# Kernel tuning notes

Hardware: AMD Instinct MI355X
Metric: run time of the kernel (lower is better)

## Reference

```python
import jax, jax.numpy as jnp
import numpy as np

B, N, D = 8, 2048, 1024
DQ, DV = 1024, 1024


def setup_inputs() -> dict:
    key = jax.random.key(0)
    ks = jax.random.split(key, 7)
    s = 1.0 / np.sqrt(D)
    return {
        "x": jax.random.normal(ks[0], (B, N, D), dtype=jnp.float32),
        "Wq": jax.random.uniform(ks[1], (D, DQ), jnp.float32, -s, s),
        "bq": jax.random.uniform(ks[2], (DQ,), jnp.float32, -s, s),
        "Wk": jax.random.uniform(ks[3], (D, DQ), jnp.float32, -s, s),
        "bk": jax.random.uniform(ks[4], (DQ,), jnp.float32, -s, s),
        "Wv": jax.random.uniform(ks[5], (D, DV), jnp.float32, -s, s),
        "bv": jax.random.uniform(ks[6], (DV,), jnp.float32, -s, s),
    }


def reference(x, Wq, bq, Wk, bk, Wv, bv):
    # Linear projections (nn.Linear: x @ W + b)
    Q = jnp.einsum("bnd,dq->bnq", x, Wq) + bq  # [B,N,DQ]
    K = jnp.einsum("bnd,dq->bnq", x, Wk) + bk  # [B,N,DQ]
    V = jnp.einsum("bnd,dv->bnv", x, Wv) + bv  # [B,N,DV]
    # NOTE: original forward does NOT apply the 1/sqrt(dk) scaling.
    scores = jnp.einsum("bnq,bmq->bnm", Q, K)  # [B,N,N]
    attn = jax.nn.softmax(scores, axis=-1)
    out = jnp.einsum("bnm,bmv->bnv", attn, V)  # [B,N,DV]
    return out
```

## Files before the change

kernel.cpp:

```cpp
#include <hip/hip_runtime.h>
#include <hip/hip_bf16.h>
#include <stdint.h>


typedef _Float16 f16;
typedef _Float16 f16x8 __attribute__((ext_vector_type(8)));
typedef _Float16 f16x4 __attribute__((ext_vector_type(4)));
typedef float f32x4 __attribute__((ext_vector_type(4)));

typedef __attribute__((address_space(3))) void lds_void;
typedef const __attribute__((address_space(1))) void gbl_void;

__device__ __forceinline__ void async16(void* l, const void* g) {
    __builtin_amdgcn_global_load_lds(
        reinterpret_cast<gbl_void*>(reinterpret_cast<uintptr_t>(g)),
        reinterpret_cast<lds_void*>(reinterpret_cast<uintptr_t>(l)),
        16, 0, 0);
}

__global__ __launch_bounds__(256) void cast_f32_f16(const float* __restrict__ x,
                                                    f16* __restrict__ y) {
    long i = (long)blockIdx.x * 256 + threadIdx.x;
    float4 v = reinterpret_cast<const float4*>(x)[i];
    f16x4 o = {(f16)v.x, (f16)v.y, (f16)v.z, (f16)v.w};
    reinterpret_cast<f16x4*>(y)[i] = o;
}

__global__ __launch_bounds__(256) void transpose_cast3(const float* __restrict__ W0,
                                                       const float* __restrict__ W1,
                                                       const float* __restrict__ W2,
                                                       f16* __restrict__ wt) {
    const float* W = blockIdx.z == 0 ? W0 : blockIdx.z == 1 ? W1 : W2;
    f16* o = wt + (long)blockIdx.z * 1024 * 1024;
    __shared__ float tile[32][33];
    int c0 = blockIdx.x * 32, r0 = blockIdx.y * 32;
    int tx = threadIdx.x, ty = threadIdx.y;
#pragma unroll
    for (int i = ty; i < 32; i += 8) tile[i][tx] = W[(long)(r0 + i) * 1024 + c0 + tx];
    __syncthreads();
#pragma unroll
    for (int i = ty; i < 32; i += 8) o[(long)(c0 + i) * 1024 + r0 + tx] = (f16)tile[tx][i];
}

template <int MODE>
__global__ __launch_bounds__(512, 2) void gemm256(
    const f16* __restrict__ A, const f16* __restrict__ Bm,
    f16* __restrict__ o16, float* __restrict__ o32,
    const float* __restrict__ bq, const float* __restrict__ bk,
    const float* __restrict__ bv,
    f16* __restrict__ Qo, f16* __restrict__ Ko, f16* __restrict__ Vto) {
    constexpr int LDA = MODE == 2 ? 2048 : 1024;
    constexpr int LDB = MODE == 2 ? 2048 : 1024;
    constexpr int NT = (MODE == 2 ? 2048 : 1024) / 64;

    __shared__ f16 sm[65536];
    char* smb = (char*)sm;

    const int tid = threadIdx.x;
    const int lane = tid & 63;
    const int wv = tid >> 6;
    const int wmi = wv >> 2;
    const int wni = wv & 3;

    const int L = blockIdx.x;
    long mBase, nBase, oOff = 0;
    int nx = 0;
    if (MODE == 0) {
        const int xcd = L & 7, j = L >> 3;
        nx = j >> 3;
        mBase = (long)(xcd * 8 + (j & 7)) * 256;
        nBase = (long)nx * 256;
    } else if (MODE == 1) {
        const int b = L & 7, j = L >> 3;
        mBase = (long)(j & 7) * 256;
        nBase = (long)(j >> 3) * 256;
        A += (long)b * 2048 * 1024;
        Bm += (long)b * 2048 * 1024;
        oOff = (long)b * 2048 * 2048;
    } else {
        const int b = L & 7, j = L >> 3;
        mBase = (long)(j & 7) * 256;
        nBase = (long)(j >> 3) * 256;
        A += (long)b * 2048 * 2048;
        Bm += (long)b * 1024 * 2048;
        oOff = (long)b * 2048 * 1024;
    }

    const int sru = tid >> 3;
    const int sck = (tid & 7) ^ (sru & 7);
    const f16* pA = A + (mBase + sru) * LDA + sck * 8;
    const f16* pB = Bm + (nBase + sru) * LDB + sck * 8;

    auto stA = [&](int bufB, int half, int t) {
        const f16* s = pA + half * 128 * LDA + t * 64;
        char* d = smb + bufB + half * 16384 + tid * 16;
        async16(d, s);
        async16(d + 8192, s + 64 * LDA);
    };
    auto stB = [&](int bufB, int half, int t) {
        const f16* s = pB + half * 128 * LDB + t * 64;
        char* d = smb + bufB + 32768 + half * 16384 + tid * 16;
        async16(d, s);
        async16(d + 8192, s + 64 * LDB);
    };

    const int pc0 = (lane >> 4) ^ (lane & 7);
    const int aBase = (wmi * 128 + (lane & 15)) * 64 + pc0 * 8;
    const int bBase = 16384 + (wni * 64 + (lane & 15)) * 64 + pc0 * 8;

    stA(0, 0, 0); stA(0, 1, 0); stB(0, 0, 0); stB(0, 1, 0);
    stA(65536, 0, 1); stA(65536, 1, 1); stB(65536, 0, 1);
    asm volatile("s_waitcnt vmcnt(6)" ::: "memory");
    __builtin_amdgcn_s_barrier();

    f32x4 acc[8][4] = {};
    for (int t = 0; t < NT; ++t) {
        const int cE = (t & 1) << 15;
        const int cB = (t & 1) << 16;
        const int nB = cB ^ 65536;
        f16x8 a0[8], a1[8], bA[2], bB[2], bC[2], bD[2];
#pragma unroll
        for (int mf = 0; mf < 8; ++mf)
            a0[mf] = *reinterpret_cast<const f16x8*>(&sm[cE + aBase + mf * 1024]);
#pragma unroll
        for (int q = 0; q < 2; ++q)
            bA[q] = *reinterpret_cast<const f16x8*>(&sm[cE + bBase + q * 1024]);
        if (t + 1 < NT) stB(nB, 1, t + 1);
        __builtin_amdgcn_s_barrier();
        asm volatile("s_waitcnt lgkmcnt(0)" ::: "memory");
        __builtin_amdgcn_sched_barrier(0);
        __builtin_amdgcn_s_setprio(1);
#pragma unroll
        for (int mf = 0; mf < 8; ++mf) {
            acc[mf][0] = __builtin_amdgcn_mfma_f32_16x16x32_f16(a0[mf], bA[0], acc[mf][0], 0, 0, 0);
            acc[mf][1] = __builtin_amdgcn_mfma_f32_16x16x32_f16(a0[mf], bA[1], acc[mf][1], 0, 0, 0);
        }
        __builtin_amdgcn_s_setprio(0);
        __builtin_amdgcn_s_barrier();
#pragma unroll
        for (int mf = 0; mf < 8; ++mf)
            a1[mf] = *reinterpret_cast<const f16x8*>(&sm[cE + ((aBase + mf * 1024) ^ 32)]);
#pragma unroll
        for (int q = 0; q < 2; ++q)
            bB[q] = *reinterpret_cast<const f16x8*>(&sm[cE + bBase + (2 + q) * 1024]);
        __builtin_amdgcn_s_barrier();
        asm volatile("s_waitcnt lgkmcnt(0)" ::: "memory");
        __builtin_amdgcn_sched_barrier(0);
        __builtin_amdgcn_s_setprio(1);
#pragma unroll
        for (int mf = 0; mf < 8; ++mf) {
            acc[mf][2] = __builtin_amdgcn_mfma_f32_16x16x32_f16(a0[mf], bB[0], acc[mf][2], 0, 0, 0);
            acc[mf][3] = __builtin_amdgcn_mfma_f32_16x16x32_f16(a0[mf], bB[1], acc[mf][3], 0, 0, 0);
        }
        __builtin_amdgcn_s_setprio(0);
        __builtin_amdgcn_s_barrier();
#pragma unroll
        for (int q = 0; q < 2; ++q)
            bC[q] = *reinterpret_cast<const f16x8*>(&sm[cE + ((bBase + q * 1024) ^ 32)]);
#pragma unroll
        for (int q = 0; q < 2; ++q)
            bD[q] = *reinterpret_cast<const f16x8*>(&sm[cE + ((bBase + (2 + q) * 1024) ^ 32)]);
        if (t + 2 < NT) { stA(cB, 0, t + 2); stA(cB, 1, t + 2); }
        __builtin_amdgcn_s_barrier();
        asm volatile("s_waitcnt lgkmcnt(0)" ::: "memory");
        __builtin_amdgcn_sched_barrier(0);
        __builtin_amdgcn_s_setprio(1);
#pragma unroll
        for (int mf = 0; mf < 8; ++mf) {
            acc[mf][0] = __builtin_amdgcn_mfma_f32_16x16x32_f16(a1[mf], bC[0], acc[mf][0], 0, 0, 0);
            acc[mf][1] = __builtin_amdgcn_mfma_f32_16x16x32_f16(a1[mf], bC[1], acc[mf][1], 0, 0, 0);
        }
        __builtin_amdgcn_s_setprio(0);
        __builtin_amdgcn_s_barrier();
        if (t + 2 < NT) stB(cB, 0, t + 2);
        __builtin_amdgcn_s_barrier();
        __builtin_amdgcn_s_setprio(1);
#pragma unroll
        for (int mf = 0; mf < 8; ++mf) {
            acc[mf][2] = __builtin_amdgcn_mfma_f32_16x16x32_f16(a1[mf], bD[0], acc[mf][2], 0, 0, 0);
            acc[mf][3] = __builtin_amdgcn_mfma_f32_16x16x32_f16(a1[mf], bD[1], acc[mf][3], 0, 0, 0);
        }
        __builtin_amdgcn_s_setprio(0);
        if (t < NT - 2) {
            asm volatile("s_waitcnt vmcnt(6)" ::: "memory");
        } else {
            asm volatile("s_waitcnt vmcnt(0)" ::: "memory");
        }
        __builtin_amdgcn_s_barrier();
    }

    const int rq = (lane >> 4) * 4;
    const int cl = lane & 15;
    if (MODE == 0) {
        const int seg = nx >> 2;
        const float* bias = seg == 0 ? bq : seg == 1 ? bk : bv;
        f16* outQK = seg == 0 ? Qo : Ko;
#pragma unroll
        for (int mf = 0; mf < 8; ++mf)
#pragma unroll
            for (int nf = 0; nf < 4; ++nf) {
                const long c = (nBase & 1023) + wni * 64 + nf * 16 + cl;
                const float bb = bias[c];
#pragma unroll
                for (int r = 0; r < 4; ++r) {
                    const long row = mBase + wmi * 128 + mf * 16 + rq + r;
                    const float v = acc[mf][nf][r] + bb;
                    if (seg < 2) {
                        outQK[row * 1024 + c] = (f16)v;
                    } else {
                        Vto[((row >> 11) * 1024 + c) * 2048 + (row & 2047)] = (f16)v;
                    }
                }
            }
    } else if (MODE == 1) {
        f16* o = o16 + oOff;
#pragma unroll
        for (int mf = 0; mf < 8; ++mf)
#pragma unroll
            for (int nf = 0; nf < 4; ++nf) {
                const long col = nBase + wni * 64 + nf * 16 + cl;
#pragma unroll
                for (int r = 0; r < 4; ++r) {
                    const long row = mBase + wmi * 128 + mf * 16 + rq + r;
                    o[row * 2048 + col] = (f16)acc[mf][nf][r];
                }
            }
    } else {
        float* o = o32 + oOff;
#pragma unroll
        for (int mf = 0; mf < 8; ++mf)
#pragma unroll
            for (int nf = 0; nf < 4; ++nf) {
                const long col = nBase + wni * 64 + nf * 16 + cl;
#pragma unroll
                for (int r = 0; r < 4; ++r) {
                    const long row = mBase + wmi * 128 + mf * 16 + rq + r;
                    o[row * 1024 + col] = acc[mf][nf][r];
                }
            }
    }
}

__global__ __launch_bounds__(256) void softmax_rows(const f16* __restrict__ S,
                                                    f16* __restrict__ P) {
    const long row = blockIdx.x;
    const int t = threadIdx.x;
    f16x8 a = reinterpret_cast<const f16x8*>(S + row * 2048)[t];
    float e[8];
    float m = -1e30f;
#pragma unroll
    for (int j = 0; j < 8; ++j) { e[j] = (float)a[j]; m = fmaxf(m, e[j]); }
#pragma unroll
    for (int o = 32; o > 0; o >>= 1) m = fmaxf(m, __shfl_down(m, o, 64));
    __shared__ float red[8];
    if ((t & 63) == 0) red[t >> 6] = m;
    __syncthreads();
    m = fmaxf(fmaxf(red[0], red[1]), fmaxf(red[2], red[3]));
    float s = 0.0f;
#pragma unroll
    for (int j = 0; j < 8; ++j) { e[j] = __expf(e[j] - m); s += e[j]; }
#pragma unroll
    for (int o = 32; o > 0; o >>= 1) s += __shfl_down(s, o, 64);
    if ((t & 63) == 0) red[4 + (t >> 6)] = s;
    __syncthreads();
    s = red[4] + red[5] + red[6] + red[7];
    float inv = 1.0f / s;
    f16x8 o;
#pragma unroll
    for (int j = 0; j < 8; ++j) o[j] = (f16)(e[j] * inv);
    reinterpret_cast<f16x8*>(P + row * 2048)[t] = o;
}

extern "C" void kernel_launch(void* const* d_in, const int* in_sizes, int n_in,
                              void* d_out, int out_size, void* d_ws, size_t ws_size,
                              hipStream_t stream) {
    const float* x  = (const float*)d_in[0];
    const float* Wq = (const float*)d_in[1];
    const float* bq = (const float*)d_in[2];
    const float* Wk = (const float*)d_in[3];
    const float* bk = (const float*)d_in[4];
    const float* Wv = (const float*)d_in[5];
    const float* bv = (const float*)d_in[6];
    float* out = (float*)d_out;
    char* ws = (char*)d_ws;

    f16* Q   = (f16*)(ws + 0);
    f16* Kb  = (f16*)(ws + 33554432);
    f16* Vt  = (f16*)(ws + 67108864);
    f16* S16 = (f16*)(ws + 100663296);
    f16* P   = (f16*)(ws + 167772160);
    f16* xh  = (f16*)(ws + 100663296);
    f16* wt  = (f16*)(ws + 134217728);

    cast_f32_f16<<<16384, 256, 0, stream>>>(x, xh);
    transpose_cast3<<<dim3(32, 32, 3), dim3(32, 8), 0, stream>>>(Wq, Wk, Wv, wt);

    gemm256<0><<<768, 512, 0, stream>>>(xh, wt, nullptr, nullptr,
                                        bq, bk, bv, Q, Kb, Vt);

    gemm256<1><<<512, 512, 0, stream>>>(Q, Kb, S16, nullptr,
                                        nullptr, nullptr, nullptr,
                                        nullptr, nullptr, nullptr);

    softmax_rows<<<16384, 256, 0, stream>>>(S16, P);

    gemm256<2><<<256, 512, 0, stream>>>(P, Vt, nullptr, out,
                                        nullptr, nullptr, nullptr,
                                        nullptr, nullptr, nullptr);
}
```

Before: 423.4 us.

## Software-pipeline LDS fragment reads with register double-buffering in GEMM main loop

Restructures the GEMM inner loop so LDS fragment loads for the next quarter-tile go into alternate register sets (aX/bX, aY/bY) while MFMAs run on the current set. The explicit lgkmcnt(0) waits and sched_barriers before each MFMA block are removed, and the first fragment of the next K tile is prefetched across the iteration boundary. Global-to-LDS async loads for tile t+2 are regrouped and the wait becomes vmcnt(0) instead of vmcnt(6). This targets LDS-latency stalls between MFMA phases. In exchange it uses more VGPRs, and the barrier and waitcnt placement is subtle, so there is a risk of races or reduced overlap of global loads.

Result: no change. 417.1 us (-1.5%).

```diff
diff --git a/kernel.cpp b/kernel.cpp
--- a/kernel.cpp
+++ b/kernel.cpp
@@ -108,84 +108,61 @@
     const int aBase = (wmi * 128 + (lane & 15)) * 64 + pc0 * 8;
     const int bBase = 16384 + (wni * 64 + (lane & 15)) * 64 + pc0 * 8;
 
+    f32x4 acc[8][4] = {};
+    f16x8 aX[4], bX[4], aY[4], bY[4];
+
+    auto rdA = [&](f16x8* dst, int cE, int mh, int ksx) {
+#pragma unroll
+        for (int i = 0; i < 4; ++i)
+            dst[i] = *reinterpret_cast<const f16x8*>(
+                &sm[cE + ((aBase + (mh * 4 + i) * 1024) ^ ksx)]);
+    };
+    auto rdB = [&](f16x8* dst, int cE, int ksx) {
+#pragma unroll
+        for (int q = 0; q < 4; ++q)
+            dst[q] = *reinterpret_cast<const f16x8*>(
+                &sm[cE + ((bBase + q * 1024) ^ ksx)]);
+    };
+    auto mm = [&](int mh, const f16x8* a, const f16x8* b) {
+        __builtin_amdgcn_s_setprio(1);
+#pragma unroll
+        for (int i = 0; i < 4; ++i)
+#pragma unroll
+            for (int nf = 0; nf < 4; ++nf)
+                acc[mh * 4 + i][nf] = __builtin_amdgcn_mfma_f32_16x16x32_f16(
+                    a[i], b[nf], acc[mh * 4 + i][nf], 0, 0, 0);
+        __builtin_amdgcn_s_setprio(0);
+    };
+
     stA(0, 0, 0); stA(0, 1, 0); stB(0, 0, 0); stB(0, 1, 0);
     stA(65536, 0, 1); stA(65536, 1, 1); stB(65536, 0, 1);
     asm volatile("s_waitcnt vmcnt(6)" ::: "memory");
     __builtin_amdgcn_s_barrier();
-
-    f32x4 acc[8][4] = {};
+    rdA(aX, 0, 0, 0); rdB(bX, 0, 0);
+
     for (int t = 0; t < NT; ++t) {
         const int cE = (t & 1) << 15;
         const int cB = (t & 1) << 16;
         const int nB = cB ^ 65536;
-        f16x8 a0[8], a1[8], bA[2], bB[2], bC[2], bD[2];
-#pragma unroll
-        for (int mf = 0; mf < 8; ++mf)
-            a0[mf] = *reinterpret_cast<const f16x8*>(&sm[cE + aBase + mf * 1024]);
-#pragma unroll
-        for (int q = 0; q < 2; ++q)
-            bA[q] = *reinterpret_cast<const f16x8*>(&sm[cE + bBase + q * 1024]);
+        rdA(aY, cE, 1, 0); rdB(bY, cE, 0);
         if (t + 1 < NT) stB(nB, 1, t + 1);
-        __builtin_amdgcn_s_barrier();
-        asm volatile("s_waitcnt lgkmcnt(0)" ::: "memory");
-        __builtin_amdgcn_sched_barrier(0);
-        __builtin_amdgcn_s_setprio(1);
-#pragma unroll
-        for (int mf = 0; mf < 8; ++mf) {
-            acc[mf][0] = __builtin_amdgcn_mfma_f32_16x16x32_f16(a0[mf], bA[0], acc[mf][0], 0, 0, 0);
-            acc[mf][1] = __builtin_amdgcn_mfma_f32_16x16x32_f16(a0[mf], bA[1], acc[mf][1], 0, 0, 0);
+        mm(0, aX, bX);
+        __builtin_amdgcn_s_barrier();
+        rdA(aX, cE, 0, 32); rdB(bX, cE, 32);
+        mm(1, aY, bY);
+        __builtin_amdgcn_s_barrier();
+        rdA(aY, cE, 1, 32); rdB(bY, cE, 32);
+        mm(0, aX, bX);
+        __builtin_amdgcn_s_barrier();
+        asm volatile("s_waitcnt vmcnt(0)" ::: "memory");
+        if (t + 1 < NT) {
+            rdA(aX, cE ^ 32768, 0, 0); rdB(bX, cE ^ 32768, 0);
+            asm volatile("s_waitcnt lgkmcnt(8)" ::: "memory");
+        } else {
+            asm volatile("s_waitcnt lgkmcnt(0)" ::: "memory");
         }
-        __builtin_amdgcn_s_setprio(0);
-        __builtin_amdgcn_s_barrier();
-#pragma unroll
-        for (int mf = 0; mf < 8; ++mf)
-            a1[mf] = *reinterpret_cast<const f16x8*>(&sm[cE + ((aBase + mf * 1024) ^ 32)]);
-#pragma unroll
-        for (int q = 0; q < 2; ++q)
-            bB[q] = *reinterpret_cast<const f16x8*>(&sm[cE + bBase + (2 + q) * 1024]);
-        __builtin_amdgcn_s_barrier();
-        asm volatile("s_waitcnt lgkmcnt(0)" ::: "memory");
-        __builtin_amdgcn_sched_barrier(0);
-        __builtin_amdgcn_s_setprio(1);
-#pragma unroll
-        for (int mf = 0; mf < 8; ++mf) {
-            acc[mf][2] = __builtin_amdgcn_mfma_f32_16x16x32_f16(a0[mf], bB[0], acc[mf][2], 0, 0, 0);
-            acc[mf][3] = __builtin_amdgcn_mfma_f32_16x16x32_f16(a0[mf], bB[1], acc[mf][3], 0, 0, 0);
-        }
-        __builtin_amdgcn_s_setprio(0);
-        __builtin_amdgcn_s_barrier();
-#pragma unroll
-        for (int q = 0; q < 2; ++q)
-            bC[q] = *reinterpret_cast<const f16x8*>(&sm[cE + ((bBase + q * 1024) ^ 32)]);
-#pragma unroll
-        for (int q = 0; q < 2; ++q)
-            bD[q] = *reinterpret_cast<const f16x8*>(&sm[cE + ((bBase + (2 + q) * 1024) ^ 32)]);
-        if (t + 2 < NT) { stA(cB, 0, t + 2); stA(cB, 1, t + 2); }
-        __builtin_amdgcn_s_barrier();
-        asm volatile("s_waitcnt lgkmcnt(0)" ::: "memory");
-        __builtin_amdgcn_sched_barrier(0);
-        __builtin_amdgcn_s_setprio(1);
-#pragma unroll
-        for (int mf = 0; mf < 8; ++mf) {
-            acc[mf][0] = __builtin_amdgcn_mfma_f32_16x16x32_f16(a1[mf], bC[0], acc[mf][0], 0, 0, 0);
-            acc[mf][1] = __builtin_amdgcn_mfma_f32_16x16x32_f16(a1[mf], bC[1], acc[mf][1], 0, 0, 0);
-        }
-        __builtin_amdgcn_s_setprio(0);
-        __builtin_amdgcn_s_barrier();
-        if (t + 2 < NT) stB(cB, 0, t + 2);
-        __builtin_amdgcn_s_barrier();
-        __builtin_amdgcn_s_setprio(1);
-#pragma unroll
-        for (int mf = 0; mf < 8; ++mf) {
-            acc[mf][2] = __builtin_amdgcn_mfma_f32_16x16x32_f16(a1[mf], bD[0], acc[mf][2], 0, 0, 0);
-            acc[mf][3] = __builtin_amdgcn_mfma_f32_16x16x32_f16(a1[mf], bD[1], acc[mf][3], 0, 0, 0);
-        }
-        __builtin_amdgcn_s_setprio(0);
-        if (t < NT - 2) {
-            asm volatile("s_waitcnt vmcnt(6)" ::: "memory");
-        } else {
-            asm volatile("s_waitcnt vmcnt(0)" ::: "memory");
-        }
+        if (t + 2 < NT) { stA(cB, 0, t + 2); stA(cB, 1, t + 2); stB(cB, 0, t + 2); }
+        mm(1, aY, bY);
         __builtin_amdgcn_s_barrier();
     }
 
```
